# Kernel tuning notes

Hardware: AMD Instinct MI355X
Metric: run time of the kernel (lower is better)

The kernel has to match this reference:

```python
import jax, jax.numpy as jnp
import numpy as np

B, N, H, HID, LOCALITY = 2, 4096, 4, 256, 30.0
VD = HID // H
F32_MAX = jnp.finfo(jnp.float32).max


def setup_inputs() -> dict:
    key = jax.random.key(0)
    k1, k2, k3, k4 = jax.random.split(key, 4)
    m_dist = jax.random.uniform(k1, (B, N, N), dtype=jnp.float32)  # pairwise distances (b,N,N)
    x = jax.random.normal(k2, (B, N, HID), dtype=jnp.float32)
    r = jax.random.normal(k3, (1, H, 1, 1), dtype=jnp.float32)  # learned per-head distance scale
    # lecun_normal: std = 1/sqrt(fan_in), fan_in = HID
    weight = jax.random.normal(k4, (H, HID, VD), dtype=jnp.float32) / np.sqrt(HID)
    return {"m_dist": m_dist, "x": x, "r": r, "weight": weight}


def reference(m_dist, x, r, weight):
    # scaled distance per head: (b,h,n,n)
    scaled = m_dist[:, None, :, :] * (r ** 2)
    # percentile-thresholded local mask (linear interpolation, per row)
    thresh = jnp.percentile(scaled, LOCALITY, axis=-1, keepdims=True, method="linear")
    scaled = jnp.where(scaled <= thresh, scaled, F32_MAX)
    att = jax.nn.softmax(-scaled, axis=-1)  # (b,h,n,n)
    value = jnp.einsum("bnj,hjk->bhnk", x, weight)  # (b,h,n,v)
    out = jnp.einsum("bhnj,bhjd->bhnd", att, value)  # (b,h,n,v)
    out = jnp.transpose(out, (0, 2, 1, 3)).reshape(out.shape[0], -1, HID)  # (b,n,hid)
    return jax.nn.gelu(out, approximate=False)
```

## Files before the change

### kernel.cpp

```cpp
#include <hip/hip_runtime.h>
#include <hip/hip_bf16.h>

#define Bc   2
#define Nc   4096
#define Hc   4
#define HIDc 256
#define VDc  64

typedef short s8v  __attribute__((ext_vector_type(8)));
typedef float f4v  __attribute__((ext_vector_type(4)));

static __device__ __forceinline__ unsigned short bf16bits(float f) {
    __hip_bfloat16 h = __float2bfloat16(f);
    return *(unsigned short*)&h;
}

__global__ __launch_bounds__(256) void front_kernel(
    const float* __restrict__ m_dist, const float* __restrict__ wgt,
    unsigned short* __restrict__ wh, unsigned short* __restrict__ wl,
    float* __restrict__ thr_out, float* __restrict__ min_out)
{
    int t = threadIdx.x, bid = blockIdx.x;

    if (bid < 128) {
        int h  = bid >> 5;
        int kt = (bid >> 3) & 3;
        int jc = bid & 7;
        int lane = t >> 2, ii = t & 3;
        #pragma unroll
        for (int u = 0; u < 2; u++) {
            int i = ii * 2 + u;
            int j = jc * 32 + (lane >> 4) * 8 + i;
            int k = kt * 16 + (lane & 15);
            float v = wgt[((size_t)h * HIDc + j) * VDc + k];
            __hip_bfloat16 hb = __float2bfloat16(v);
            float hf = __bfloat162float(hb);
            size_t o = ((((size_t)h * 4 + kt) * 8 + jc) * 64 + lane) * 8 + i;
            wh[o] = *(unsigned short*)&hb;
            wl[o] = bf16bits(v - hf);
        }
        return;
    }

    __shared__ unsigned int hist[1024];
    __shared__ float wredf[4];
    __shared__ unsigned int wsum[4];
    __shared__ unsigned int wscan[4];
    __shared__ int b0s, b1s;
    __shared__ unsigned int c0s;
    __shared__ unsigned int ncand;
    __shared__ float cand[256];
    __shared__ float s0s, s1s;

    size_t rowid = bid - 128;
    const float* row = m_dist + rowid * Nc;

    float4 vals[4];
    float lmin = 1e30f;
    #pragma unroll
    for (int i = 0; i < 4; i++) {
        float4 v = ((const float4*)row)[t + i * 256];
        vals[i] = v;
        lmin = fminf(lmin, fminf(fminf(v.x, v.y), fminf(v.z, v.w)));
    }
    #pragma unroll
    for (int o = 32; o > 0; o >>= 1) lmin = fminf(lmin, __shfl_xor(lmin, o));
    if ((t & 63) == 0) wredf[t >> 6] = lmin;

    const unsigned int R0 = 1228u, R1 = 1229u;
    float wlo = 0.25f, whi = 0.35f;
    int b0 = 0, b1 = 0;
    unsigned int C0 = 0;

    for (;;) {
        float wscale = 1024.0f / (whi - wlo);

        for (int i = t; i < 1024; i += 256) hist[i] = 0u;
        if (t == 0) ncand = 0u;
        __syncthreads();

        unsigned int cb = 0;
        #pragma unroll
        for (int i = 0; i < 4; i++) {
            float a[4] = {vals[i].x, vals[i].y, vals[i].z, vals[i].w};
            #pragma unroll
            for (int j = 0; j < 4; j++) {
                float v = a[j];
                if (v < wlo) {
                    cb++;
                } else {
                    int bx = (int)((v - wlo) * wscale);
                    if (bx < 1024) atomicAdd(&hist[bx], 1u);
                }
            }
        }
        #pragma unroll
        for (int o = 32; o > 0; o >>= 1) cb += __shfl_xor(cb, o);
        if ((t & 63) == 0) wsum[t >> 6] = cb;
        __syncthreads();
        unsigned int Cb = wsum[0] + wsum[1] + wsum[2] + wsum[3];

        unsigned int c[4], csum = 0;
        #pragma unroll
        for (int j = 0; j < 4; j++) { c[j] = hist[t * 4 + j]; csum += c[j]; }
        unsigned int inc = csum;
        #pragma unroll
        for (int o = 1; o < 64; o <<= 1) {
            unsigned int nv = __shfl_up(inc, o);
            if ((t & 63) >= o) inc += nv;
        }
        if ((t & 63) == 63) wscan[t >> 6] = inc;
        __syncthreads();
        unsigned int wpref = 0;
        for (int wv = 0; wv < (t >> 6); wv++) wpref += wscan[wv];
        unsigned int T = wscan[0] + wscan[1] + wscan[2] + wscan[3];
        unsigned int P = Cb + wpref + inc - csum;

        unsigned int cum = P;
        #pragma unroll
        for (int j = 0; j < 4; j++) {
            unsigned int lo = cum, hi = cum + c[j];
            if (R0 >= lo && R0 < hi) { b0s = t * 4 + j; c0s = lo; }
            if (R1 >= lo && R1 < hi) { b1s = t * 4 + j; }
            cum = hi;
        }
        __syncthreads();

        if (Cb <= R0 && R1 < Cb + T) { b0 = b0s; b1 = b1s; C0 = c0s; break; }
        wlo = 0.0f; whi = 1.001f;
    }

    float wscale = 1024.0f / (whi - wlo);
    #pragma unroll
    for (int i = 0; i < 4; i++) {
        float a[4] = {vals[i].x, vals[i].y, vals[i].z, vals[i].w};
        #pragma unroll
        for (int j = 0; j < 4; j++) {
            float v = a[j];
            if (v >= wlo) {
                int bx = (int)((v - wlo) * wscale);
                if (bx >= b0 && bx <= b1) {
                    unsigned int p = atomicAdd(&ncand, 1u);
                    if (p < 256u) cand[p] = v;
                }
            }
        }
    }
    __syncthreads();
    unsigned int nc = min(ncand, 256u);
    if ((unsigned int)t < nc) {
        float v = cand[t];
        unsigned int rk = C0;
        for (unsigned int j = 0; j < nc; j++) {
            float u = cand[j];
            rk += (u < v || (u == v && j < (unsigned int)t)) ? 1u : 0u;
        }
        if (rk == R0) s0s = v;
        if (rk == R1) s1s = v;
    }
    __syncthreads();
    if (t == 0) {
        thr_out[rowid] = 0.5f * (s0s + s1s);
        min_out[rowid] = fminf(fminf(wredf[0], wredf[1]), fminf(wredf[2], wredf[3]));
    }
}

__global__ __launch_bounds__(256) void value_kernel(
    const float* __restrict__ x,
    const unsigned short* __restrict__ wh, const unsigned short* __restrict__ wl,
    unsigned short* __restrict__ vt_g)
{
    int t  = threadIdx.x;
    int bid = blockIdx.x;
    int nt = bid & 63;
    int h  = (bid >> 6) & 3;
    int b  = bid >> 8;
    int n0 = nt * 64;

    int w = t >> 6, lane = t & 63, q4 = lane >> 4, m16 = lane & 15;
    int nb = n0 + w * 16;

    const float* xp = x + ((size_t)(b * Nc + nb + m16)) * HIDc + q4 * 8;

    f4v acc[4];
    #pragma unroll
    for (int kt = 0; kt < 4; kt++) acc[kt] = (f4v){0.f, 0.f, 0.f, 0.f};

    #pragma unroll
    for (int jc = 0; jc < 8; jc++) {
        float4 xv0 = *(const float4*)(xp + jc * 32);
        float4 xv1 = *(const float4*)(xp + jc * 32 + 4);
        float f[8] = {xv0.x, xv0.y, xv0.z, xv0.w, xv1.x, xv1.y, xv1.z, xv1.w};
        union { s8v v; unsigned short u[8]; } hs, ls;
        #pragma unroll
        for (int i = 0; i < 8; i++) {
            __hip_bfloat16 hb = __float2bfloat16(f[i]);
            float hf = __bfloat162float(hb);
            hs.u[i] = *(unsigned short*)&hb;
            ls.u[i] = bf16bits(f[i] - hf);
        }
        #pragma unroll
        for (int kt = 0; kt < 4; kt++) {
            size_t ao = (((size_t)(h * 4 + kt) * 8 + jc) << 9) + lane * 8;
            s8v ah = *(const s8v*)(wh + ao);
            s8v al = *(const s8v*)(wl + ao);
            acc[kt] = __builtin_amdgcn_mfma_f32_16x16x32_bf16(ah, hs.v, acc[kt], 0, 0, 0);
            acc[kt] = __builtin_amdgcn_mfma_f32_16x16x32_bf16(al, hs.v, acc[kt], 0, 0, 0);
            acc[kt] = __builtin_amdgcn_mfma_f32_16x16x32_bf16(ah, ls.v, acc[kt], 0, 0, 0);
        }
    }

    unsigned short* vg = vt_g + (((size_t)b * Hc + h) * VDc) * Nc;
    #pragma unroll
    for (int kt = 0; kt < 4; kt++) {
        #pragma unroll
        for (int rg = 0; rg < 4; rg++) {
            int k = kt * 16 + q4 * 4 + rg;
            vg[(size_t)k * Nc + nb + m16] = bf16bits(acc[kt][rg]);
        }
    }
}

#define NT 64
#define JT 32

__global__ __launch_bounds__(1024, 8) void attn_kernel(
    const float* __restrict__ m_dist, const float* __restrict__ rr,
    const unsigned short* __restrict__ vt_g,
    const float* __restrict__ thr_g, const float* __restrict__ min_g,
    float* __restrict__ Op, float* __restrict__ Zp, int jlen)
{
    __shared__ float msL[3][NT * JT];
    __shared__ unsigned short vtL[3][Hc * VDc * JT];

    int t = threadIdx.x;
    const int nblk = Bc * (Nc / NT);
    int js = blockIdx.x / nblk;
    int rb = blockIdx.x - js * nblk;
    int b  = rb >> 6;
    int n0 = (rb & 63) * NT;
    int j0 = js * jlen;

    int lane = t & 63, q = lane >> 4, m16 = lane & 15;
    int w = t >> 6;
    int h = w & 3, rq = w >> 2;
    int row = rq * 16 + m16;

    float mn = min_g[b * Nc + n0 + row];
    float thm = thr_g[b * Nc + n0 + row];
    float rv = rr[h];
    float cc = -(rv * rv) * 1.4426950408889634f;
    float nmncc = -mn * cc;

    f4v acc[4];
    #pragma unroll
    for (int ct = 0; ct < 4; ct++) acc[ct] = (f4v){0.f, 0.f, 0.f, 0.f};
    float zacc = 0.f;

    const float* mbase = m_dist + ((size_t)b * Nc + n0) * Nc + j0;
    const unsigned short* vtb = vt_g + ((size_t)b * Hc * VDc) * Nc + j0;

    const float* msrc = mbase + (size_t)(t >> 3) * Nc + (((t & 7) ^ ((t >> 3) & 7)) << 2);
    const unsigned short* vsrc = vtb + (size_t)(t >> 2) * Nc + (((t & 3) ^ ((t >> 2) & 3)) << 3);

    int s7 = m16 & 7;
    int a0o = row * JT + (((q * 2 + 0) ^ s7) << 2);
    int a1o = row * JT + (((q * 2 + 1) ^ s7) << 2);
    int bco = (q ^ (m16 & 3)) << 3;
    const int hoff = h * VDc * JT;

    int niter = jlen / JT;

    #define STAGE(k, bi) do {                                                  \
        int jo_ = (k) * JT;                                                    \
        if (t < 512)                                                           \
            __builtin_amdgcn_global_load_lds(                                  \
                (const __attribute__((address_space(1))) void*)(msrc + jo_),   \
                (__attribute__((address_space(3))) void*)                      \
                    ((char*)&msL[bi][0] + (size_t)t * 16),                     \
                16, 0, 0);                                                     \
        __builtin_amdgcn_global_load_lds(                                      \
            (const __attribute__((address_space(1))) void*)(vsrc + jo_),       \
            (__attribute__((address_space(3))) void*)                          \
                ((char*)&vtL[bi][0] + (size_t)t * 16),                         \
            16, 0, 0);                                                         \
    } while (0)

    STAGE(0, 0);
    STAGE(1, 1);

    int bi = 0;
    for (int it = 0; it < niter; ++it) {
        if (it + 1 < niter) {
            if (w < 8) { asm volatile("s_waitcnt vmcnt(2)" ::: "memory"); }
            else       { asm volatile("s_waitcnt vmcnt(1)" ::: "memory"); }
        } else {
            asm volatile("s_waitcnt vmcnt(0)" ::: "memory");
        }
        __builtin_amdgcn_sched_barrier(0);
        __builtin_amdgcn_s_barrier();
        __builtin_amdgcn_sched_barrier(0);

        if (it + 2 < niter) {
            int bn = bi + 2; if (bn >= 3) bn -= 3;
            STAGE(it + 2, bn);
        }

        const float* msp = &msL[bi][0];
        const unsigned short* vb = &vtL[bi][hoff];
        float4 a0 = *(const float4*)(msp + a0o);
        float4 a1 = *(const float4*)(msp + a1o);
        float w0 = (a0.x <= thm) ? __builtin_amdgcn_exp2f(__builtin_fmaf(a0.x, cc, nmncc)) : 0.f;
        float w1 = (a0.y <= thm) ? __builtin_amdgcn_exp2f(__builtin_fmaf(a0.y, cc, nmncc)) : 0.f;
        float w2 = (a0.z <= thm) ? __builtin_amdgcn_exp2f(__builtin_fmaf(a0.z, cc, nmncc)) : 0.f;
        float w3 = (a0.w <= thm) ? __builtin_amdgcn_exp2f(__builtin_fmaf(a0.w, cc, nmncc)) : 0.f;
        float w4 = (a1.x <= thm) ? __builtin_amdgcn_exp2f(__builtin_fmaf(a1.x, cc, nmncc)) : 0.f;
        float w5 = (a1.y <= thm) ? __builtin_amdgcn_exp2f(__builtin_fmaf(a1.y, cc, nmncc)) : 0.f;
        float w6 = (a1.z <= thm) ? __builtin_amdgcn_exp2f(__builtin_fmaf(a1.z, cc, nmncc)) : 0.f;
        float w7 = (a1.w <= thm) ? __builtin_amdgcn_exp2f(__builtin_fmaf(a1.w, cc, nmncc)) : 0.f;
        zacc += ((w0 + w1) + (w2 + w3)) + ((w4 + w5) + (w6 + w7));
        union { s8v v; __hip_bfloat162 h2[4]; } afu;
        afu.h2[0] = __float22bfloat162_rn((float2){w0, w1});
        afu.h2[1] = __float22bfloat162_rn((float2){w2, w3});
        afu.h2[2] = __float22bfloat162_rn((float2){w4, w5});
        afu.h2[3] = __float22bfloat162_rn((float2){w6, w7});
        #pragma unroll
        for (int ct = 0; ct < 4; ct++) {
            int brow = ct * 16 + m16;
            s8v bf = *(const s8v*)(vb + brow * JT + bco);
            acc[ct] = __builtin_amdgcn_mfma_f32_16x16x32_bf16(afu.v, bf, acc[ct], 0, 0, 0);
        }
        bi = bi + 1; if (bi >= 3) bi -= 3;
    }
    #undef STAGE

    zacc += __shfl_xor(zacc, 16);
    zacc += __shfl_xor(zacc, 32);
    if (q == 0)
        Zp[(((size_t)js * Bc + b) * Hc + h) * Nc + n0 + row] = zacc;

    #pragma unroll
    for (int ct = 0; ct < 4; ct++) {
        #pragma unroll
        for (int rg = 0; rg < 4; rg++) {
            int nl = rq * 16 + q * 4 + rg;
            Op[(((size_t)js * Bc + b) * Nc + n0 + nl) * HIDc + h * VDc + ct * 16 + m16]
                = acc[ct][rg];
        }
    }
}

__global__ __launch_bounds__(256) void combine_kernel(
    const float* __restrict__ Op, const float* __restrict__ Zp,
    float* __restrict__ out, int S)
{
    int g = blockIdx.x * 256 + threadIdx.x;
    int c4 = g & 63;
    int n  = (g >> 6) & (Nc - 1);
    int b  = g >> 18;
    int h  = c4 >> 4;

    float z = 0.f;
    float4 v = {0.f, 0.f, 0.f, 0.f};
    for (int s = 0; s < S; s++) {
        z += Zp[(((size_t)s * Bc + b) * Hc + h) * Nc + n];
        float4 p = *(const float4*)&Op[(((size_t)s * Bc + b) * Nc + n) * HIDc + c4 * 4];
        v.x += p.x; v.y += p.y; v.z += p.z; v.w += p.w;
    }
    float iz = 1.0f / z;
    float4 o;
    float u;
    u = v.x * iz; o.x = 0.5f * u * (1.0f + erff(u * 0.7071067811865476f));
    u = v.y * iz; o.y = 0.5f * u * (1.0f + erff(u * 0.7071067811865476f));
    u = v.z * iz; o.z = 0.5f * u * (1.0f + erff(u * 0.7071067811865476f));
    u = v.w * iz; o.w = 0.5f * u * (1.0f + erff(u * 0.7071067811865476f));
    *(float4*)&out[(((size_t)b * Nc + n) * HIDc) + c4 * 4] = o;
}

extern "C" void kernel_launch(void* const* d_in, const int* in_sizes, int n_in,
                              void* d_out, int out_size, void* d_ws, size_t ws_size,
                              hipStream_t stream) {
    const float* m_dist = (const float*)d_in[0];
    const float* x      = (const float*)d_in[1];
    const float* r      = (const float*)d_in[2];
    const float* weight = (const float*)d_in[3];
    float* out = (float*)d_out;

    char* ws = (char*)d_ws;
    const size_t MB = 1024 * 1024;
    unsigned short* vt = (unsigned short*)ws;
    float* thr = (float*)(ws + 4 * MB);
    float* mn  = (float*)(ws + 4 * MB + 32 * 1024);
    float* Zp  = (float*)(ws + 4 * MB + 64 * 1024);
    float* Op  = (float*)(ws + 5 * MB);

    const size_t OpSz = (size_t)Bc * Nc * HIDc * 4;
    int S = 4;
    if (ws_size < 6 * MB + 4 * OpSz) S = 2;
    if (ws_size < 6 * MB + 2 * OpSz) S = 1;
    int jlen = Nc / S;

    char* pb = ws + 5 * MB + (size_t)S * OpSz;
    unsigned short* wh = (unsigned short*)pb;
    unsigned short* wl = (unsigned short*)(pb + 128 * 1024);

    front_kernel<<<128 + Bc * Nc, 256, 0, stream>>>(m_dist, weight, wh, wl, thr, mn);
    value_kernel<<<512, 256, 0, stream>>>(x, wh, wl, vt);
    attn_kernel<<<S * Bc * (Nc / NT), 1024, 0, stream>>>(m_dist, r, vt, thr, mn, Op, Zp, jlen);
    combine_kernel<<<(Bc * Nc * HIDc) / 1024, 256, 0, stream>>>(Op, Zp, out, S);
}
```

Baseline: 263.4 us.

## Halve attention block threads, give each wave two row tiles, load distances directly

The attention kernel now runs 512 threads per block, and each wave handles two 16-row tiles that share the same B fragment of V from LDS, so each V load feeds two MFMAs. The distance matrix is no longer staged through LDS. Each lane loads its own rows into registers one iteration ahead, and only the V tiles keep the triple-buffered async LDS path. The loop is unrolled by two with rotating buffers. This cuts LDS traffic and barrier work per FLOP but raises register pressure, and the direct global reads of m_dist may be less coalesced, with less latency hiding.

Result: slower. 299.4 us (+13.7%).

```diff
diff --git a/kernel.cpp b/kernel.cpp
--- a/kernel.cpp
+++ b/kernel.cpp
@@ -224,13 +224,12 @@
 #define NT 64
 #define JT 32
 
-__global__ __launch_bounds__(1024, 8) void attn_kernel(
+__global__ __launch_bounds__(512, 4) void attn_kernel(
     const float* __restrict__ m_dist, const float* __restrict__ rr,
     const unsigned short* __restrict__ vt_g,
     const float* __restrict__ thr_g, const float* __restrict__ min_g,
     float* __restrict__ Op, float* __restrict__ Zp, int jlen)
 {
-    __shared__ float msL[3][NT * JT];
     __shared__ unsigned short vtL[3][Hc * VDc * JT];
 
     int t = threadIdx.x;
@@ -243,109 +242,157 @@
 
     int lane = t & 63, q = lane >> 4, m16 = lane & 15;
     int w = t >> 6;
-    int h = w & 3, rq = w >> 2;
-    int row = rq * 16 + m16;
-
-    float mn = min_g[b * Nc + n0 + row];
-    float thm = thr_g[b * Nc + n0 + row];
+    int h = w & 3, rhalf = w >> 2;
+    int row0 = rhalf * 32 + m16;
+    int row1 = row0 + 16;
+
+    float mn0 = min_g[b * Nc + n0 + row0];
+    float mn1 = min_g[b * Nc + n0 + row1];
+    float th0 = thr_g[b * Nc + n0 + row0];
+    float th1 = thr_g[b * Nc + n0 + row1];
     float rv = rr[h];
     float cc = -(rv * rv) * 1.4426950408889634f;
-    float nmncc = -mn * cc;
-
-    f4v acc[4];
-    #pragma unroll
-    for (int ct = 0; ct < 4; ct++) acc[ct] = (f4v){0.f, 0.f, 0.f, 0.f};
-    float zacc = 0.f;
-
-    const float* mbase = m_dist + ((size_t)b * Nc + n0) * Nc + j0;
+    float nm0 = -mn0 * cc, nm1 = -mn1 * cc;
+
+    f4v acc0[4], acc1[4];
+    #pragma unroll
+    for (int ct = 0; ct < 4; ct++) {
+        acc0[ct] = (f4v){0.f, 0.f, 0.f, 0.f};
+        acc1[ct] = (f4v){0.f, 0.f, 0.f, 0.f};
+    }
+    float z0 = 0.f, z1 = 0.f;
+
+    const float* mb0 = m_dist + ((size_t)(b * Nc + n0 + row0)) * Nc + j0 + q * 8;
+    const float* mb1 = mb0 + (size_t)16 * Nc;
+
     const unsigned short* vtb = vt_g + ((size_t)b * Hc * VDc) * Nc + j0;
-
-    const float* msrc = mbase + (size_t)(t >> 3) * Nc + (((t & 7) ^ ((t >> 3) & 7)) << 2);
-    const unsigned short* vsrc = vtb + (size_t)(t >> 2) * Nc + (((t & 3) ^ ((t >> 2) & 3)) << 3);
-
-    int s7 = m16 & 7;
-    int a0o = row * JT + (((q * 2 + 0) ^ s7) << 2);
-    int a1o = row * JT + (((q * 2 + 1) ^ s7) << 2);
+    int vrow = t >> 2;
+    const unsigned short* vsrc  = vtb + (size_t)vrow * Nc + (((t & 3) ^ (vrow & 3)) << 3);
+    const unsigned short* vsrc2 = vsrc + (size_t)128 * Nc;
+
     int bco = (q ^ (m16 & 3)) << 3;
     const int hoff = h * VDc * JT;
 
     int niter = jlen / JT;
 
-    #define STAGE(k, bi) do {                                                  \
-        int jo_ = (k) * JT;                                                    \
-        if (t < 512)                                                           \
-            __builtin_amdgcn_global_load_lds(                                  \
-                (const __attribute__((address_space(1))) void*)(msrc + jo_),   \
-                (__attribute__((address_space(3))) void*)                      \
-                    ((char*)&msL[bi][0] + (size_t)t * 16),                     \
-                16, 0, 0);                                                     \
+    char* L0 = (char*)&vtL[0][0];
+    char* L1 = (char*)&vtL[1][0];
+    char* L2 = (char*)&vtL[2][0];
+
+    #define STAGE(k, LB) do {                                                  \
+        size_t jo_ = (size_t)(k) * JT;                                         \
         __builtin_amdgcn_global_load_lds(                                      \
             (const __attribute__((address_space(1))) void*)(vsrc + jo_),       \
-            (__attribute__((address_space(3))) void*)                          \
-                ((char*)&vtL[bi][0] + (size_t)t * 16),                         \
+            (__attribute__((address_space(3))) void*)((LB) + (size_t)t * 16),  \
+            16, 0, 0);                                                         \
+        __builtin_amdgcn_global_load_lds(                                      \
+            (const __attribute__((address_space(1))) void*)(vsrc2 + jo_),      \
+            (__attribute__((address_space(3))) void*)((LB) + 8192 + (size_t)t * 16), \
             16, 0, 0);                                                         \
     } while (0)
 
-    STAGE(0, 0);
-    STAGE(1, 1);
-
-    int bi = 0;
-    for (int it = 0; it < niter; ++it) {
-        if (it + 1 < niter) {
-            if (w < 8) { asm volatile("s_waitcnt vmcnt(2)" ::: "memory"); }
-            else       { asm volatile("s_waitcnt vmcnt(1)" ::: "memory"); }
-        } else {
-            asm volatile("s_waitcnt vmcnt(0)" ::: "memory");
-        }
+    #define RLOAD(k, r00, r01, r10, r11) do {                                  \
+        size_t jo_ = (size_t)(k) * JT;                                         \
+        r00 = *(const float4*)(mb0 + jo_);                                     \
+        r01 = *(const float4*)(mb0 + jo_ + 4);                                 \
+        r10 = *(const float4*)(mb1 + jo_);                                     \
+        r11 = *(const float4*)(mb1 + jo_ + 4);                                 \
+    } while (0)
+
+    #define COMPUTE(r00, r01, r10, r11, LB) do {                               \
+        const unsigned short* vb_ = (const unsigned short*)(LB) + hoff;        \
+        float w0 = (r00.x <= th0) ? __builtin_amdgcn_exp2f(__builtin_fmaf(r00.x, cc, nm0)) : 0.f; \
+        float w1 = (r00.y <= th0) ? __builtin_amdgcn_exp2f(__builtin_fmaf(r00.y, cc, nm0)) : 0.f; \
+        float w2 = (r00.z <= th0) ? __builtin_amdgcn_exp2f(__builtin_fmaf(r00.z, cc, nm0)) : 0.f; \
+        float w3 = (r00.w <= th0) ? __builtin_amdgcn_exp2f(__builtin_fmaf(r00.w, cc, nm0)) : 0.f; \
+        float w4 = (r01.x <= th0) ? __builtin_amdgcn_exp2f(__builtin_fmaf(r01.x, cc, nm0)) : 0.f; \
+        float w5 = (r01.y <= th0) ? __builtin_amdgcn_exp2f(__builtin_fmaf(r01.y, cc, nm0)) : 0.f; \
+        float w6 = (r01.z <= th0) ? __builtin_amdgcn_exp2f(__builtin_fmaf(r01.z, cc, nm0)) : 0.f; \
+        float w7 = (r01.w <= th0) ? __builtin_amdgcn_exp2f(__builtin_fmaf(r01.w, cc, nm0)) : 0.f; \
+        z0 += ((w0 + w1) + (w2 + w3)) + ((w4 + w5) + (w6 + w7));               \
+        float v0 = (r10.x <= th1) ? __builtin_amdgcn_exp2f(__builtin_fmaf(r10.x, cc, nm1)) : 0.f; \
+        float v1 = (r10.y <= th1) ? __builtin_amdgcn_exp2f(__builtin_fmaf(r10.y, cc, nm1)) : 0.f; \
+        float v2 = (r10.z <= th1) ? __builtin_amdgcn_exp2f(__builtin_fmaf(r10.z, cc, nm1)) : 0.f; \
+        float v3 = (r10.w <= th1) ? __builtin_amdgcn_exp2f(__builtin_fmaf(r10.w, cc, nm1)) : 0.f; \
+        float v4 = (r11.x <= th1) ? __builtin_amdgcn_exp2f(__builtin_fmaf(r11.x, cc, nm1)) : 0.f; \
+        float v5 = (r11.y <= th1) ? __builtin_amdgcn_exp2f(__builtin_fmaf(r11.y, cc, nm1)) : 0.f; \
+        float v6 = (r11.z <= th1) ? __builtin_amdgcn_exp2f(__builtin_fmaf(r11.z, cc, nm1)) : 0.f; \
+        float v7 = (r11.w <= th1) ? __builtin_amdgcn_exp2f(__builtin_fmaf(r11.w, cc, nm1)) : 0.f; \
+        z1 += ((v0 + v1) + (v2 + v3)) + ((v4 + v5) + (v6 + v7));               \
+        union { s8v v; __hip_bfloat162 h2[4]; } af0, af1;                      \
+        af0.h2[0] = __float22bfloat162_rn((float2){w0, w1});                   \
+        af0.h2[1] = __float22bfloat162_rn((float2){w2, w3});                   \
+        af0.h2[2] = __float22bfloat162_rn((float2){w4, w5});                   \
+        af0.h2[3] = __float22bfloat162_rn((float2){w6, w7});                   \
+        af1.h2[0] = __float22bfloat162_rn((float2){v0, v1});                   \
+        af1.h2[1] = __float22bfloat162_rn((float2){v2, v3});                   \
+        af1.h2[2] = __float22bfloat162_rn((float2){v4, v5});                   \
+        af1.h2[3] = __float22bfloat162_rn((float2){v6, v7});                   \
+        _Pragma("unroll")                                                      \
+        for (int ct_ = 0; ct_ < 4; ct_++) {                                    \
+            int brow_ = ct_ * 16 + m16;                                        \
+            s8v bf_ = *(const s8v*)(vb_ + brow_ * JT + bco);                   \
+            acc0[ct_] = __builtin_amdgcn_mfma_f32_16x16x32_bf16(af0.v, bf_, acc0[ct_], 0, 0, 0); \
+            acc1[ct_] = __builtin_amdgcn_mfma_f32_16x16x32_bf16(af1.v, bf_, acc1[ct_], 0, 0, 0); \
+        }                                                                      \
+    } while (0)
+
+    float4 rA00, rA01, rA10, rA11;
+    float4 rB00, rB01, rB10, rB11;
+
+    STAGE(0, L0);
+    __builtin_amdgcn_sched_barrier(0);
+    RLOAD(0, rA00, rA01, rA10, rA11);
+    __builtin_amdgcn_sched_barrier(0);
+    STAGE(1, L1);
+    __builtin_amdgcn_sched_barrier(0);
+
+    for (int it = 0; it < niter; it += 2) {
+        asm volatile("s_waitcnt vmcnt(2)" ::: "memory");
         __builtin_amdgcn_sched_barrier(0);
         __builtin_amdgcn_s_barrier();
         __builtin_amdgcn_sched_barrier(0);
-
+        RLOAD(it + 1, rB00, rB01, rB10, rB11);
+        __builtin_amdgcn_sched_barrier(0);
+        if (it + 2 < niter) STAGE(it + 2, L2);
+        __builtin_amdgcn_sched_barrier(0);
+        COMPUTE(rA00, rA01, rA10, rA11, L0);
+
+        if (it + 2 < niter) { asm volatile("s_waitcnt vmcnt(2)" ::: "memory"); }
+        else                { asm volatile("s_waitcnt vmcnt(0)" ::: "memory"); }
+        __builtin_amdgcn_sched_barrier(0);
+        __builtin_amdgcn_s_barrier();
+        __builtin_amdgcn_sched_barrier(0);
         if (it + 2 < niter) {
-            int bn = bi + 2; if (bn >= 3) bn -= 3;
-            STAGE(it + 2, bn);
-        }
-
-        const float* msp = &msL[bi][0];
-        const unsigned short* vb = &vtL[bi][hoff];
-        float4 a0 = *(const float4*)(msp + a0o);
-        float4 a1 = *(const float4*)(msp + a1o);
-        float w0 = (a0.x <= thm) ? __builtin_amdgcn_exp2f(__builtin_fmaf(a0.x, cc, nmncc)) : 0.f;
-        float w1 = (a0.y <= thm) ? __builtin_amdgcn_exp2f(__builtin_fmaf(a0.y, cc, nmncc)) : 0.f;
-        float w2 = (a0.z <= thm) ? __builtin_amdgcn_exp2f(__builtin_fmaf(a0.z, cc, nmncc)) : 0.f;
-        float w3 = (a0.w <= thm) ? __builtin_amdgcn_exp2f(__builtin_fmaf(a0.w, cc, nmncc)) : 0.f;
-        float w4 = (a1.x <= thm) ? __builtin_amdgcn_exp2f(__builtin_fmaf(a1.x, cc, nmncc)) : 0.f;
-        float w5 = (a1.y <= thm) ? __builtin_amdgcn_exp2f(__builtin_fmaf(a1.y, cc, nmncc)) : 0.f;
-        float w6 = (a1.z <= thm) ? __builtin_amdgcn_exp2f(__builtin_fmaf(a1.z, cc, nmncc)) : 0.f;
-        float w7 = (a1.w <= thm) ? __builtin_amdgcn_exp2f(__builtin_fmaf(a1.w, cc, nmncc)) : 0.f;
-        zacc += ((w0 + w1) + (w2 + w3)) + ((w4 + w5) + (w6 + w7));
-        union { s8v v; __hip_bfloat162 h2[4]; } afu;
-        afu.h2[0] = __float22bfloat162_rn((float2){w0, w1});
-        afu.h2[1] = __float22bfloat162_rn((float2){w2, w3});
-        afu.h2[2] = __float22bfloat162_rn((float2){w4, w5});
-        afu.h2[3] = __float22bfloat162_rn((float2){w6, w7});
-        #pragma unroll
-        for (int ct = 0; ct < 4; ct++) {
-            int brow = ct * 16 + m16;
-            s8v bf = *(const s8v*)(vb + brow * JT + bco);
-            acc[ct] = __builtin_amdgcn_mfma_f32_16x16x32_bf16(afu.v, bf, acc[ct], 0, 0, 0);
-        }
-        bi = bi + 1; if (bi >= 3) bi -= 3;
+            RLOAD(it + 2, rA00, rA01, rA10, rA11);
+            __builtin_amdgcn_sched_barrier(0);
+            if (it + 3 < niter) STAGE(it + 3, L0);
+            __builtin_amdgcn_sched_barrier(0);
+        }
+        COMPUTE(rB00, rB01, rB10, rB11, L1);
+
+        char* tmp = L0; L0 = L2; L2 = L1; L1 = tmp;
     }
     #undef STAGE
-
-    zacc += __shfl_xor(zacc, 16);
-    zacc += __shfl_xor(zacc, 32);
-    if (q == 0)
-        Zp[(((size_t)js * Bc + b) * Hc + h) * Nc + n0 + row] = zacc;
+    #undef RLOAD
+    #undef COMPUTE
+
+    z0 += __shfl_xor(z0, 16); z0 += __shfl_xor(z0, 32);
+    z1 += __shfl_xor(z1, 16); z1 += __shfl_xor(z1, 32);
+    if (q == 0) {
+        size_t zb = (((size_t)js * Bc + b) * Hc + h) * Nc + n0;
+        Zp[zb + row0] = z0;
+        Zp[zb + row1] = z1;
+    }
 
     #pragma unroll
     for (int ct = 0; ct < 4; ct++) {
         #pragma unroll
         for (int rg = 0; rg < 4; rg++) {
-            int nl = rq * 16 + q * 4 + rg;
-            Op[(((size_t)js * Bc + b) * Nc + n0 + nl) * HIDc + h * VDc + ct * 16 + m16]
-                = acc[ct][rg];
+            int nl = rhalf * 32 + q * 4 + rg;
+            size_t ob = (((size_t)js * Bc + b) * Nc + n0 + nl) * HIDc + h * VDc + ct * 16 + m16;
+            Op[ob] = acc0[ct][rg];
+            Op[ob + (size_t)16 * HIDc] = acc1[ct][rg];
         }
     }
 }
@@ -406,6 +453,6 @@
 
     front_kernel<<<128 + Bc * Nc, 256, 0, stream>>>(m_dist, weight, wh, wl, thr, mn);
     value_kernel<<<512, 256, 0, stream>>>(x, wh, wl, vt);
-    attn_kernel<<<S * Bc * (Nc / NT), 1024, 0, stream>>>(m_dist, r, vt, thr, mn, Op, Zp, jlen);
+    attn_kernel<<<S * Bc * (Nc / NT), 512, 0, stream>>>(m_dist, r, vt, thr, mn, Op, Zp, jlen);
     combine_kernel<<<(Bc * Nc * HIDc) / 1024, 256, 0, stream>>>(Op, Zp, out, S);
 }
```
